# Performance work log

Hardware: AMD Instinct MI355X
Metric: run time of the kernel (lower is better)

The kernel has to match this reference:

```python
import jax, jax.numpy as jnp
import numpy as np

N, E, D, H = 20000, 320000, 300, 2
NEG_SLOPE = 0.2  # PyG GATConv default LeakyReLU slope


def setup_inputs() -> dict:
    key = jax.random.key(0)
    ks = jax.random.split(key, 8)
    return {
        "x": jax.random.normal(ks[0], (N, D), dtype=jnp.float32),
        "edge_index": jax.random.randint(ks[1], (2, E), 0, N, dtype=jnp.int64),
        "W": jax.random.normal(ks[2], (D, H, D), dtype=jnp.float32) * 0.05,
        "att_src": jax.random.normal(ks[3], (H, D), dtype=jnp.float32) * 0.05,
        "att_dst": jax.random.normal(ks[4], (H, D), dtype=jnp.float32) * 0.05,
        "bias": jax.random.normal(ks[5], (D,), dtype=jnp.float32) * 0.05,
        "lin_w": jax.random.normal(ks[6], (D, 1), dtype=jnp.float32) * 0.05,
        "lin_b": jax.random.normal(ks[7], (1,), dtype=jnp.float32) * 0.05,
    }


def reference(x, edge_index, W, att_src, att_dst, bias, lin_w, lin_b):
    n = x.shape[0]
    # add self-loops (PyG GATConv default)
    loops = jnp.arange(n, dtype=edge_index.dtype)
    src = jnp.concatenate([edge_index[0], loops])  # [E+N]
    dst = jnp.concatenate([edge_index[1], loops])
    # per-head linear projection: [N, H, D]
    xp = jnp.einsum('nd,dhe->nhe', x, W)
    # per-node attention logits [N, H]
    a_src = jnp.sum(xp * att_src, axis=-1)
    a_dst = jnp.sum(xp * att_dst, axis=-1)
    # per-edge score, LeakyReLU, segment softmax over incoming edges of dst
    e = jax.nn.leaky_relu(a_src[src] + a_dst[dst], NEG_SLOPE)  # [Et, H]
    emax = jax.ops.segment_max(e, dst, num_segments=n)  # self-loops ensure non-empty
    ee = jnp.exp(e - emax[dst])
    denom = jax.ops.segment_sum(ee, dst, num_segments=n)
    alpha = ee / denom[dst]  # [Et, H]
    # weighted scatter-add aggregation
    msg = xp[src] * alpha[:, :, None]  # [Et, H, D]
    out = jax.ops.segment_sum(msg, dst, num_segments=n)  # [N, H, D]
    out = out.mean(axis=1) + bias  # concat=False -> head average, then bias
    out = jax.nn.relu(out)
    return out @ lin_w + lin_b  # [N, 1]
```

## Files before the change

kernel.cpp:

```cpp
#include <hip/hip_runtime.h>
#include <math.h>

#define Nn 20000
#define Ee 320000
#define Dd 300
#define Hh 2
#define Cc 600
#define KP 320
#define MP 20096
#define NP 640
#define SQ 640

typedef _Float16 f16;
typedef __attribute__((ext_vector_type(8))) _Float16 f16x8;
typedef __attribute__((ext_vector_type(4))) _Float16 f16x4;
typedef __attribute__((ext_vector_type(4))) float f32x4;

__device__ __forceinline__ float lrelu(float x) { return x > 0.f ? x : 0.2f * x; }

__global__ __launch_bounds__(256) void k_pre2(const float* __restrict__ W,
                                              const float* __restrict__ att_src,
                                              const float* __restrict__ att_dst,
                                              f16* __restrict__ Wh, float* __restrict__ vatt) {
  int idx = blockIdx.x * 256 + threadIdx.x;
  {
    int c = idx % NP, k0 = (idx / NP) * 4;
    f16x4 h;
#pragma unroll
    for (int j = 0; j < 4; ++j) {
      int k = k0 + j;
      h[j] = (f16)((k < Dd && c < Cc) ? W[(size_t)k * Cc + c] : 0.f);
    }
    *(f16x4*)(Wh + (size_t)c * KP + k0) = h;
  }
  int wid = idx >> 6, ln = idx & 63;
  if (wid < Dd) {
    float s0 = 0.f, s1 = 0.f, t0 = 0.f, t1 = 0.f;
    for (int e = ln; e < Dd; e += 64) {
      float w0 = W[(size_t)wid * Cc + e];
      float w1 = W[(size_t)wid * Cc + Dd + e];
      s0 += w0 * att_src[e];  s1 += w1 * att_src[Dd + e];
      t0 += w0 * att_dst[e];  t1 += w1 * att_dst[Dd + e];
    }
    for (int o = 32; o > 0; o >>= 1) {
      s0 += __shfl_down(s0, o, 64); s1 += __shfl_down(s1, o, 64);
      t0 += __shfl_down(t0, o, 64); t1 += __shfl_down(t1, o, 64);
    }
    if (ln == 0) {
      vatt[wid * 4 + 0] = s0; vatt[wid * 4 + 1] = s1;
      vatt[wid * 4 + 2] = t0; vatt[wid * 4 + 3] = t1;
    }
  }
}

__global__ __launch_bounds__(256) void k_pre1(const float* __restrict__ x,
                                              const float* __restrict__ vatt,
                                              f16* __restrict__ xh,
                                              float* __restrict__ a_src, float* __restrict__ a_dst,
                                              int* __restrict__ cnt) {
  int gid = blockIdx.x * 256 + threadIdx.x;
  if (gid < Nn) cnt[gid] = 0;
  int wv = threadIdx.x >> 6, ln = threadIdx.x & 63;
  int n = blockIdx.x * 4 + wv;
  if (n >= MP) return;
  if (n >= Nn) {
#pragma unroll
    for (int k = 0; k < 5; ++k) xh[(size_t)n * KP + ln + 64 * k] = (f16)0.f;
    return;
  }
  const float* xr = x + (size_t)n * Dd;
  float s0 = 0.f, s1 = 0.f, t0 = 0.f, t1 = 0.f;
#pragma unroll
  for (int k = 0; k < 5; ++k) {
    int d = ln + 64 * k;
    float xv = 0.f;
    if (d < Dd) {
      xv = xr[d];
      float4 vv = *(const float4*)(vatt + d * 4);
      s0 += xv * vv.x; s1 += xv * vv.y; t0 += xv * vv.z; t1 += xv * vv.w;
    }
    xh[(size_t)n * KP + d] = (f16)xv;
  }
  for (int o = 32; o > 0; o >>= 1) {
    s0 += __shfl_down(s0, o, 64); s1 += __shfl_down(s1, o, 64);
    t0 += __shfl_down(t0, o, 64); t1 += __shfl_down(t1, o, 64);
  }
  if (ln == 0) {
    a_src[n * 2 + 0] = s0; a_src[n * 2 + 1] = s1;
    a_dst[n * 2 + 0] = t0; a_dst[n * 2 + 1] = t1;
  }
}

__global__ __launch_bounds__(256) void k_mm(const f16* __restrict__ xh, const f16* __restrict__ Wh,
                                            f16* __restrict__ xq) {
  __shared__ __align__(16) f16 Ash[128][40];
  __shared__ __align__(16) f16 Bsh[64][40];
  int m0 = blockIdx.x * 128, n0 = blockIdx.y * 64;
  int tid = threadIdx.x, wv = tid >> 6, lane = tid & 63;
  int srow = tid >> 2, skq = (tid & 3) * 8;
  int akq = (lane >> 4) * 8;
  f32x4 acc[2][4] = {};
  for (int ks = 0; ks < KP / 32; ++ks) {
    f16x8 va0 = *(const f16x8*)(xh + (size_t)(m0 + srow) * KP + ks * 32 + skq);
    f16x8 va1 = *(const f16x8*)(xh + (size_t)(m0 + 64 + srow) * KP + ks * 32 + skq);
    f16x8 vb  = *(const f16x8*)(Wh + (size_t)(n0 + srow) * KP + ks * 32 + skq);
    __syncthreads();
    *(f16x8*)&Ash[srow][skq]      = va0;
    *(f16x8*)&Ash[64 + srow][skq] = va1;
    *(f16x8*)&Bsh[srow][skq]      = vb;
    __syncthreads();
    f16x8 fa0 = *(const f16x8*)&Ash[32 * wv + (lane & 15)][akq];
    f16x8 fa1 = *(const f16x8*)&Ash[32 * wv + 16 + (lane & 15)][akq];
#pragma unroll
    for (int nt = 0; nt < 4; ++nt) {
      f16x8 fb = *(const f16x8*)&Bsh[16 * nt + (lane & 15)][akq];
      acc[0][nt] = __builtin_amdgcn_mfma_f32_16x16x32_f16(fa0, fb, acc[0][nt], 0, 0, 0);
      acc[1][nt] = __builtin_amdgcn_mfma_f32_16x16x32_f16(fa1, fb, acc[1][nt], 0, 0, 0);
    }
  }
#pragma unroll
  for (int g = 0; g < 2; ++g) {
#pragma unroll
    for (int nt = 0; nt < 4; ++nt) {
      int col = n0 + 16 * nt + (lane & 15);
      if (col < Cc) {
        int rbase = m0 + 32 * wv + 16 * g + ((lane >> 4) * 4);
#pragma unroll
        for (int i = 0; i < 4; ++i) {
          int row = rbase + i;
          if (row < Nn) xq[(size_t)row * SQ + col] = (f16)acc[g][nt][i];
        }
      }
    }
  }
}

__global__ void k_hist(const int* __restrict__ ei, int* __restrict__ cnt) {
  int e = blockIdx.x * 256 + threadIdx.x;
  if (e < Ee) atomicAdd(&cnt[ei[Ee + e]], 1);
}

__global__ __launch_bounds__(1024) void k_scan(const int* __restrict__ cnt,
                                               int* __restrict__ offs, int* __restrict__ cur) {
  __shared__ int wsum[16];
  int t = threadIdx.x, wv = t >> 6, ln = t & 63;
  int i0 = t * 20;
  int v[20];
  int tot = 0;
  if (i0 < Nn) {
    const int4* p = (const int4*)(cnt + i0);
#pragma unroll
    for (int q = 0; q < 5; ++q) {
      int4 w = p[q];
      v[4 * q] = w.x; v[4 * q + 1] = w.y; v[4 * q + 2] = w.z; v[4 * q + 3] = w.w;
    }
#pragma unroll
    for (int j = 0; j < 20; ++j) tot += v[j];
  }
  int s = tot;
  for (int o = 1; o < 64; o <<= 1) {
    int u = __shfl_up(s, o, 64);
    if (ln >= o) s += u;
  }
  if (ln == 63) wsum[wv] = s;
  __syncthreads();
  if (wv == 0) {
    int w = (ln < 16) ? wsum[ln] : 0;
    for (int o = 1; o < 16; o <<= 1) {
      int u = __shfl_up(w, o, 64);
      if (ln >= o) w += u;
    }
    if (ln < 16) wsum[ln] = w;
  }
  __syncthreads();
  if (i0 < Nn) {
    int run = (wv > 0 ? wsum[wv - 1] : 0) + (s - tot);
#pragma unroll
    for (int j = 0; j < 20; ++j) {
      offs[i0 + j] = run;
      cur[i0 + j] = run;
      run += v[j];
    }
  }
  if (t == 0) offs[Nn] = wsum[15];
}

__global__ void k_scatter(const int* __restrict__ ei, int* __restrict__ cur,
                          int* __restrict__ srt) {
  int e = blockIdx.x * 256 + threadIdx.x;
  if (e < Ee) {
    int s = ei[e], d = ei[Ee + e];
    int pos = atomicAdd(&cur[d], 1);
    srt[pos] = s;
  }
}

__global__ __launch_bounds__(256) void k_agg(const f16* __restrict__ xq,
    const float* __restrict__ a_src, const float* __restrict__ a_dst,
    const int* __restrict__ offs, const int* __restrict__ srt,
    const float* __restrict__ bias, const float* __restrict__ lin_w,
    const float* __restrict__ lin_b, float* __restrict__ out) {
  __shared__ float sAgg[4][600];
  int tid = threadIdx.x, wv = tid >> 6, ln = tid & 63;
  int n = blockIdx.x * 4 + wv;
  int beg = offs[n], deg = offs[n + 1] - beg;
  float2 adv = *(const float2*)(a_dst + 2 * n);
  float2 asv = *(const float2*)(a_src + 2 * n);
  float se0 = lrelu(asv.x + adv.x), se1 = lrelu(asv.y + adv.y);

  float m0 = se0, m1 = se1, s0 = 0.f, s1 = 0.f;
  int ss = -1; float ee0 = 0.f, ee1 = 0.f;
  for (int base = 0; base < deg; base += 64) {
    if (ln < deg - base) {
      int s = srt[beg + base + ln];
      float2 av = *(const float2*)(a_src + 2 * s);
      ss = s; ee0 = lrelu(av.x + adv.x); ee1 = lrelu(av.y + adv.y);
      if (ee0 > m0) { s0 *= __expf(m0 - ee0); m0 = ee0; }
      s0 += __expf(ee0 - m0);
      if (ee1 > m1) { s1 *= __expf(m1 - ee1); m1 = ee1; }
      s1 += __expf(ee1 - m1);
    }
  }
  for (int o = 32; o > 0; o >>= 1) {
    float om = __shfl_xor(m0, o, 64), os = __shfl_xor(s0, o, 64);
    float nm = fmaxf(m0, om);
    s0 = s0 * __expf(m0 - nm) + os * __expf(om - nm); m0 = nm;
    om = __shfl_xor(m1, o, 64); os = __shfl_xor(s1, o, 64);
    nm = fmaxf(m1, om);
    s1 = s1 * __expf(m1 - nm) + os * __expf(om - nm); m1 = nm;
  }
  { float nm = fmaxf(m0, se0); s0 = s0 * __expf(m0 - nm) + __expf(se0 - nm); m0 = nm; }
  { float nm = fmaxf(m1, se1); s1 = s1 * __expf(m1 - nm) + __expf(se1 - nm); m1 = nm; }
  float inv0 = 1.f / s0, inv1 = 1.f / s1;

  float acc[12] = {};
  auto addrow = [&](const f16* row, float p0, float p1) {
#pragma unroll
    for (int k = 0; k < 3; ++k) {
      int c = 4 * ln + 256 * k;
      if (c < Cc) {
        f16x4 hv = *(const f16x4*)(row + c);
        float p = (c < Dd) ? p0 : p1;
        acc[4 * k + 0] += p * (float)hv[0];
        acc[4 * k + 1] += p * (float)hv[1];
        acc[4 * k + 2] += p * (float)hv[2];
        acc[4 * k + 3] += p * (float)hv[3];
      }
    }
  };

  if (deg <= 64) {
    float p0 = __expf(ee0 - m0) * inv0, p1 = __expf(ee1 - m1) * inv1;
#pragma unroll 2
    for (int j = 0; j < deg; ++j) {
      int s = __shfl(ss, j, 64);
      float q0 = __shfl(p0, j, 64), q1 = __shfl(p1, j, 64);
      addrow(xq + (size_t)s * SQ, q0, q1);
    }
  } else {
    for (int base = 0; base < deg; base += 64) {
      int cnt2 = min(64, deg - base);
      float p0 = 0.f, p1 = 0.f; int s2 = -1;
      if (ln < cnt2) {
        int s = srt[beg + base + ln];
        float2 av = *(const float2*)(a_src + 2 * s);
        s2 = s;
        p0 = __expf(lrelu(av.x + adv.x) - m0) * inv0;
        p1 = __expf(lrelu(av.y + adv.y) - m1) * inv1;
      }
#pragma unroll 2
      for (int j = 0; j < cnt2; ++j) {
        int s = __shfl(s2, j, 64);
        float q0 = __shfl(p0, j, 64), q1 = __shfl(p1, j, 64);
        addrow(xq + (size_t)s * SQ, q0, q1);
      }
    }
  }
  addrow(xq + (size_t)n * SQ, __expf(se0 - m0) * inv0, __expf(se1 - m1) * inv1);

#pragma unroll
  for (int k = 0; k < 3; ++k) {
    int c = 4 * ln + 256 * k;
    if (c < Cc) {
#pragma unroll
      for (int j = 0; j < 4; ++j) sAgg[wv][c + j] = acc[4 * k + j];
    }
  }
  __syncthreads();

  float part = 0.f;
#pragma unroll
  for (int k = 0; k < 5; ++k) {
    int d = ln + 64 * k;
    if (d < Dd) {
      float v = 0.5f * (sAgg[wv][d] + sAgg[wv][d + Dd]) + bias[d];
      v = fmaxf(v, 0.f);
      part += v * lin_w[d];
    }
  }
  for (int o = 32; o > 0; o >>= 1) part += __shfl_xor(part, o, 64);
  if (ln == 0) out[n] = part + lin_b[0];
}

extern "C" void kernel_launch(void* const* d_in, const int* in_sizes, int n_in,
                              void* d_out, int out_size, void* d_ws, size_t ws_size,
                              hipStream_t stream) {
  const float* x       = (const float*)d_in[0];
  const int*   ei      = (const int*)d_in[1];
  const float* W       = (const float*)d_in[2];
  const float* att_src = (const float*)d_in[3];
  const float* att_dst = (const float*)d_in[4];
  const float* bias    = (const float*)d_in[5];
  const float* lin_w   = (const float*)d_in[6];
  const float* lin_b   = (const float*)d_in[7];
  float* out = (float*)d_out;

  char* ws = (char*)d_ws;
  size_t off = 0;
  auto alloc = [&](size_t bytes) {
    void* p = ws + off;
    off = (off + bytes + 255) & ~(size_t)255;
    return p;
  };
  f16*   xq    = (f16*)alloc((size_t)Nn * SQ * 2);
  f16*   xh    = (f16*)alloc((size_t)MP * KP * 2);
  f16*   Wh    = (f16*)alloc((size_t)NP * KP * 2);
  float* vatt  = (float*)alloc((size_t)Dd * 4 * 4);
  float* a_src = (float*)alloc((size_t)Nn * Hh * 4);
  float* a_dst = (float*)alloc((size_t)Nn * Hh * 4);
  int*   cnt   = (int*)alloc((size_t)Nn * 4);
  int*   offs  = (int*)alloc((size_t)(Nn + 1) * 4);
  int*   cur   = (int*)alloc((size_t)Nn * 4);
  int*   srt   = (int*)alloc((size_t)Ee * 4);

  k_pre2<<<NP * (KP / 4) / 256, 256, 0, stream>>>(W, att_src, att_dst, Wh, vatt);
  k_pre1<<<MP / 4, 256, 0, stream>>>(x, vatt, xh, a_src, a_dst, cnt);
  k_mm<<<dim3(MP / 128, NP / 64), 256, 0, stream>>>(xh, Wh, xq);
  k_hist<<<(Ee + 255) / 256, 256, 0, stream>>>(ei, cnt);
  k_scan<<<1, 1024, 0, stream>>>(cnt, offs, cur);
  k_scatter<<<(Ee + 255) / 256, 256, 0, stream>>>(ei, cur, srt);
  k_agg<<<Nn / 4, 256, 0, stream>>>(xq, a_src, a_dst, offs, srt, bias, lin_w, lin_b, out);
}
```

Measured before the change: 221.2 us.

## Fuse histogram into pre1, retile GEMM with direct-to-LDS loads, drop softmax max pass

Moves the count zeroing into k_pre2 and the destination histogram into k_pre1, removing the separate k_hist launch. Rewrites the projection GEMM to 128x128 tiles that load global memory straight into swizzled LDS via global_load_lds, with 4x4 MFMA accumulators per wave. The aggregation kernel drops the online max-subtracted softmax and uses plain exp sums, which saves a pass and the shuffle-based max merge. The exp without max subtraction could overflow for large logits, although the small weight scales here make that unlikely.

```diff
diff --git a/kernel.cpp b/kernel.cpp
--- a/kernel.cpp
+++ b/kernel.cpp
@@ -18,11 +18,18 @@
 
 __device__ __forceinline__ float lrelu(float x) { return x > 0.f ? x : 0.2f * x; }
 
+#define GLDS16(src, dst)                                                            \
+  __builtin_amdgcn_global_load_lds(                                                 \
+      (const __attribute__((address_space(1))) unsigned int*)(src),                 \
+      (__attribute__((address_space(3))) unsigned int*)(dst), 16, 0, 0)
+
 __global__ __launch_bounds__(256) void k_pre2(const float* __restrict__ W,
                                               const float* __restrict__ att_src,
                                               const float* __restrict__ att_dst,
-                                              f16* __restrict__ Wh, float* __restrict__ vatt) {
+                                              f16* __restrict__ Wh, float* __restrict__ vatt,
+                                              int* __restrict__ cnt) {
   int idx = blockIdx.x * 256 + threadIdx.x;
+  if (idx < Nn) cnt[idx] = 0;
   {
     int c = idx % NP, k0 = (idx / NP) * 4;
     f16x4 h;
@@ -55,11 +62,12 @@
 
 __global__ __launch_bounds__(256) void k_pre1(const float* __restrict__ x,
                                               const float* __restrict__ vatt,
+                                              const int* __restrict__ ei,
                                               f16* __restrict__ xh,
                                               float* __restrict__ a_src, float* __restrict__ a_dst,
                                               int* __restrict__ cnt) {
   int gid = blockIdx.x * 256 + threadIdx.x;
-  if (gid < Nn) cnt[gid] = 0;
+  if (gid < Ee) atomicAdd(&cnt[ei[Ee + gid]], 1);
   int wv = threadIdx.x >> 6, ln = threadIdx.x & 63;
   int n = blockIdx.x * 4 + wv;
   if (n >= MP) return;
@@ -93,51 +101,58 @@
 
 __global__ __launch_bounds__(256) void k_mm(const f16* __restrict__ xh, const f16* __restrict__ Wh,
                                             f16* __restrict__ xq) {
-  __shared__ __align__(16) f16 Ash[128][40];
-  __shared__ __align__(16) f16 Bsh[64][40];
-  int m0 = blockIdx.x * 128, n0 = blockIdx.y * 64;
+  __shared__ __align__(16) f16 As[128 * 32];
+  __shared__ __align__(16) f16 Bs[128 * 32];
+  int m0 = blockIdx.x * 128, n0 = blockIdx.y * 128;
   int tid = threadIdx.x, wv = tid >> 6, lane = tid & 63;
-  int srow = tid >> 2, skq = (tid & 3) * 8;
-  int akq = (lane >> 4) * 8;
-  f32x4 acc[2][4] = {};
+  int wr = wv >> 1, wc = wv & 1;
+
+  int r0a = 32 * wv + (lane >> 2);
+  int ca  = ((lane & 3) ^ ((r0a >> 1) & 3)) * 8;
+  int r0b = r0a + 16;
+  int cb  = ((lane & 3) ^ ((r0b >> 1) & 3)) * 8;
+
+  f32x4 acc[4][4] = {};
   for (int ks = 0; ks < KP / 32; ++ks) {
-    f16x8 va0 = *(const f16x8*)(xh + (size_t)(m0 + srow) * KP + ks * 32 + skq);
-    f16x8 va1 = *(const f16x8*)(xh + (size_t)(m0 + 64 + srow) * KP + ks * 32 + skq);
-    f16x8 vb  = *(const f16x8*)(Wh + (size_t)(n0 + srow) * KP + ks * 32 + skq);
     __syncthreads();
-    *(f16x8*)&Ash[srow][skq]      = va0;
-    *(f16x8*)&Ash[64 + srow][skq] = va1;
-    *(f16x8*)&Bsh[srow][skq]      = vb;
+    GLDS16(xh + (size_t)(m0 + r0a) * KP + ks * 32 + ca, As + (32 * wv) * 32);
+    GLDS16(xh + (size_t)(m0 + r0b) * KP + ks * 32 + cb, As + (32 * wv + 16) * 32);
+    GLDS16(Wh + (size_t)(n0 + r0a) * KP + ks * 32 + ca, Bs + (32 * wv) * 32);
+    GLDS16(Wh + (size_t)(n0 + r0b) * KP + ks * 32 + cb, Bs + (32 * wv + 16) * 32);
     __syncthreads();
-    f16x8 fa0 = *(const f16x8*)&Ash[32 * wv + (lane & 15)][akq];
-    f16x8 fa1 = *(const f16x8*)&Ash[32 * wv + 16 + (lane & 15)][akq];
-#pragma unroll
-    for (int nt = 0; nt < 4; ++nt) {
-      f16x8 fb = *(const f16x8*)&Bsh[16 * nt + (lane & 15)][akq];
-      acc[0][nt] = __builtin_amdgcn_mfma_f32_16x16x32_f16(fa0, fb, acc[0][nt], 0, 0, 0);
-      acc[1][nt] = __builtin_amdgcn_mfma_f32_16x16x32_f16(fa1, fb, acc[1][nt], 0, 0, 0);
-    }
-  }
-#pragma unroll
-  for (int g = 0; g < 2; ++g) {
-#pragma unroll
-    for (int nt = 0; nt < 4; ++nt) {
-      int col = n0 + 16 * nt + (lane & 15);
+
+    f16x8 af[4], bf[4];
+#pragma unroll
+    for (int i = 0; i < 4; ++i) {
+      int rA = wr * 64 + i * 16 + (lane & 15);
+      int sA = (lane >> 4) ^ ((rA >> 1) & 3);
+      af[i] = *(const f16x8*)&As[rA * 32 + sA * 8];
+      int rB = wc * 64 + i * 16 + (lane & 15);
+      int sB = (lane >> 4) ^ ((rB >> 1) & 3);
+      bf[i] = *(const f16x8*)&Bs[rB * 32 + sB * 8];
+    }
+#pragma unroll
+    for (int i = 0; i < 4; ++i)
+#pragma unroll
+      for (int j = 0; j < 4; ++j)
+        acc[i][j] = __builtin_amdgcn_mfma_f32_16x16x32_f16(af[i], bf[j], acc[i][j], 0, 0, 0);
+  }
+
+#pragma unroll
+  for (int i = 0; i < 4; ++i) {
+#pragma unroll
+    for (int j = 0; j < 4; ++j) {
+      int col = n0 + wc * 64 + j * 16 + (lane & 15);
       if (col < Cc) {
-        int rbase = m0 + 32 * wv + 16 * g + ((lane >> 4) * 4);
-#pragma unroll
-        for (int i = 0; i < 4; ++i) {
-          int row = rbase + i;
-          if (row < Nn) xq[(size_t)row * SQ + col] = (f16)acc[g][nt][i];
+        int rbase = m0 + wr * 64 + i * 16 + ((lane >> 4) * 4);
+#pragma unroll
+        for (int r = 0; r < 4; ++r) {
+          int row = rbase + r;
+          if (row < Nn) xq[(size_t)row * SQ + col] = (f16)acc[i][j][r];
         }
       }
     }
   }
-}
-
-__global__ void k_hist(const int* __restrict__ ei, int* __restrict__ cnt) {
-  int e = blockIdx.x * 256 + threadIdx.x;
-  if (e < Ee) atomicAdd(&cnt[ei[Ee + e]], 1);
 }
 
 __global__ __launch_bounds__(1024) void k_scan(const int* __restrict__ cnt,
@@ -207,31 +222,7 @@
   float2 adv = *(const float2*)(a_dst + 2 * n);
   float2 asv = *(const float2*)(a_src + 2 * n);
   float se0 = lrelu(asv.x + adv.x), se1 = lrelu(asv.y + adv.y);
-
-  float m0 = se0, m1 = se1, s0 = 0.f, s1 = 0.f;
-  int ss = -1; float ee0 = 0.f, ee1 = 0.f;
-  for (int base = 0; base < deg; base += 64) {
-    if (ln < deg - base) {
-      int s = srt[beg + base + ln];
-      float2 av = *(const float2*)(a_src + 2 * s);
-      ss = s; ee0 = lrelu(av.x + adv.x); ee1 = lrelu(av.y + adv.y);
-      if (ee0 > m0) { s0 *= __expf(m0 - ee0); m0 = ee0; }
-      s0 += __expf(ee0 - m0);
-      if (ee1 > m1) { s1 *= __expf(m1 - ee1); m1 = ee1; }
-      s1 += __expf(ee1 - m1);
-    }
-  }
-  for (int o = 32; o > 0; o >>= 1) {
-    float om = __shfl_xor(m0, o, 64), os = __shfl_xor(s0, o, 64);
-    float nm = fmaxf(m0, om);
-    s0 = s0 * __expf(m0 - nm) + os * __expf(om - nm); m0 = nm;
-    om = __shfl_xor(m1, o, 64); os = __shfl_xor(s1, o, 64);
-    nm = fmaxf(m1, om);
-    s1 = s1 * __expf(m1 - nm) + os * __expf(om - nm); m1 = nm;
-  }
-  { float nm = fmaxf(m0, se0); s0 = s0 * __expf(m0 - nm) + __expf(se0 - nm); m0 = nm; }
-  { float nm = fmaxf(m1, se1); s1 = s1 * __expf(m1 - nm) + __expf(se1 - nm); m1 = nm; }
-  float inv0 = 1.f / s0, inv1 = 1.f / s1;
+  float sw0 = __expf(se0), sw1 = __expf(se1);
 
   float acc[12] = {};
   auto addrow = [&](const f16* row, float p0, float p1) {
@@ -250,14 +241,43 @@
   };
 
   if (deg <= 64) {
-    float p0 = __expf(ee0 - m0) * inv0, p1 = __expf(ee1 - m1) * inv1;
-#pragma unroll 2
+    int ss = -1; float e0 = 0.f, e1 = 0.f;
+    if (ln < deg) {
+      int s = srt[beg + ln];
+      float2 av = *(const float2*)(a_src + 2 * s);
+      ss = s;
+      e0 = __expf(lrelu(av.x + adv.x));
+      e1 = __expf(lrelu(av.y + adv.y));
+    }
+    float t0 = e0, t1 = e1;
+    for (int o = 32; o > 0; o >>= 1) {
+      t0 += __shfl_xor(t0, o, 64);
+      t1 += __shfl_xor(t1, o, 64);
+    }
+    float inv0 = 1.f / (t0 + sw0), inv1 = 1.f / (t1 + sw1);
+    float p0 = e0 * inv0, p1 = e1 * inv1;
+#pragma unroll 4
     for (int j = 0; j < deg; ++j) {
       int s = __shfl(ss, j, 64);
       float q0 = __shfl(p0, j, 64), q1 = __shfl(p1, j, 64);
       addrow(xq + (size_t)s * SQ, q0, q1);
     }
+    addrow(xq + (size_t)n * SQ, sw0 * inv0, sw1 * inv1);
   } else {
+    float t0 = 0.f, t1 = 0.f;
+    for (int base = 0; base < deg; base += 64) {
+      if (ln < deg - base) {
+        int s = srt[beg + base + ln];
+        float2 av = *(const float2*)(a_src + 2 * s);
+        t0 += __expf(lrelu(av.x + adv.x));
+        t1 += __expf(lrelu(av.y + adv.y));
+      }
+    }
+    for (int o = 32; o > 0; o >>= 1) {
+      t0 += __shfl_xor(t0, o, 64);
+      t1 += __shfl_xor(t1, o, 64);
+    }
+    float inv0 = 1.f / (t0 + sw0), inv1 = 1.f / (t1 + sw1);
     for (int base = 0; base < deg; base += 64) {
       int cnt2 = min(64, deg - base);
       float p0 = 0.f, p1 = 0.f; int s2 = -1;
@@ -265,18 +285,18 @@
         int s = srt[beg + base + ln];
         float2 av = *(const float2*)(a_src + 2 * s);
         s2 = s;
-        p0 = __expf(lrelu(av.x + adv.x) - m0) * inv0;
-        p1 = __expf(lrelu(av.y + adv.y) - m1) * inv1;
-      }
-#pragma unroll 2
+        p0 = __expf(lrelu(av.x + adv.x)) * inv0;
+        p1 = __expf(lrelu(av.y + adv.y)) * inv1;
+      }
+#pragma unroll 4
       for (int j = 0; j < cnt2; ++j) {
         int s = __shfl(s2, j, 64);
         float q0 = __shfl(p0, j, 64), q1 = __shfl(p1, j, 64);
         addrow(xq + (size_t)s * SQ, q0, q1);
       }
     }
-  }
-  addrow(xq + (size_t)n * SQ, __expf(se0 - m0) * inv0, __expf(se1 - m1) * inv1);
+    addrow(xq + (size_t)n * SQ, sw0 * inv0, sw1 * inv1);
+  }
 
 #pragma unroll
   for (int k = 0; k < 3; ++k) {
@@ -333,10 +353,9 @@
   int*   cur   = (int*)alloc((size_t)Nn * 4);
   int*   srt   = (int*)alloc((size_t)Ee * 4);
 
-  k_pre2<<<NP * (KP / 4) / 256, 256, 0, stream>>>(W, att_src, att_dst, Wh, vatt);
-  k_pre1<<<MP / 4, 256, 0, stream>>>(x, vatt, xh, a_src, a_dst, cnt);
-  k_mm<<<dim3(MP / 128, NP / 64), 256, 0, stream>>>(xh, Wh, xq);
-  k_hist<<<(Ee + 255) / 256, 256, 0, stream>>>(ei, cnt);
+  k_pre2<<<NP * (KP / 4) / 256, 256, 0, stream>>>(W, att_src, att_dst, Wh, vatt, cnt);
+  k_pre1<<<MP / 4, 256, 0, stream>>>(x, vatt, ei, xh, a_src, a_dst, cnt);
+  k_mm<<<dim3(MP / 128, NP / 128), 256, 0, stream>>>(xh, Wh, xq);
   k_scan<<<1, 1024, 0, stream>>>(cnt, offs, cur);
   k_scatter<<<(Ee + 255) / 256, 256, 0, stream>>>(ei, cur, srt);
   k_agg<<<Nn / 4, 256, 0, stream>>>(xq, a_src, a_dst, offs, srt, bias, lin_w, lin_b, out);
```

Result: faster. 214.3 us (-3.2%).
